# Kernel tuning notes

Hardware: AMD Instinct MI355X
Metric: run time of the kernel (lower is better)

Reference implementation:

```python
import jax, jax.numpy as jnp
import numpy as np

H = 450    # hidden_size (JTNN default)
LAT = 56   # latent_size (tree_vec dim)
V = 780    # vocab size
T = 1024   # n_trees
L = 24     # nodes per tree (path topology)


def _tree_meta(Ln):
    # forward edge i: (i, i+1) eid=i ; reverse edge i: (i+1, i) eid=(Ln-1)+i
    n_f = Ln - 1
    eids, preds, srcs, dsts, labels = [], [], [], [], []
    for i in range(n_f):  # forward DFS steps
        eids.append(i); srcs.append(i); dsts.append(i + 1)
        preds.append(i - 1 if i > 0 else -1); labels.append(0)
    for k in range(n_f):  # backtrack DFS steps (reverse edges, deepest first)
        i = n_f - 1 - k
        eids.append(n_f + i); srcs.append(i + 1); dsts.append(i)
        preds.append(n_f + i + 1 if i < n_f - 1 else -1); labels.append(1)
    # incoming edges of the dst node v (for the node 'pull' h = sum of m)
    in1 = [d - 1 if d > 0 else -1 for d in dsts]
    in2 = [n_f + d if d < n_f else -1 for d in dsts]
    meta = [np.asarray(a, np.int32) for a in (eids, preds, srcs, dsts, in1, in2)]
    return meta, np.asarray(labels, np.float32)


def setup_inputs():
    key = jax.random.key(0)
    ks = jax.random.split(key, 12)
    s = 0.05
    return {
        "wid": jax.random.randint(ks[0], (T, L), 0, V, dtype=jnp.int32),
        "tree_vec": jax.random.normal(ks[1], (T, LAT), jnp.float32),
        "emb": jax.random.normal(ks[2], (V, H)) * s,
        "W_w": jax.random.normal(ks[3], (H + LAT, H)) * s, "W_b": jnp.zeros((H,)),
        "U_w": jax.random.normal(ks[4], (2 * H + LAT, H)) * s, "U_b": jnp.zeros((H,)),
        "Wo_w": jax.random.normal(ks[5], (H, V)) * s, "Wo_b": jnp.zeros((V,)),
        "Us_w": jax.random.normal(ks[6], (H, 1)) * s, "Us_b": jnp.zeros((1,)),
        "Wz_w": jax.random.normal(ks[7], (2 * H, H)) * s, "Wz_b": jnp.zeros((H,)),
        "Wr_w": jax.random.normal(ks[8], (H, H)) * s,
        "Ur_w": jax.random.normal(ks[9], (H, H)) * s, "Ur_b": jnp.zeros((H,)),
        "Wh_w": jax.random.normal(ks[10], (2 * H, H)) * s, "Wh_b": jnp.zeros((H,)),
    }


def reference(wid, tree_vec, emb, W_w, W_b, U_w, U_b, Wo_w, Wo_b, Us_w, Us_b,
              Wz_w, Wz_b, Wr_w, Ur_w, Ur_b, Wh_w, Wh_b):
    Tn, Ln = wid.shape
    n_f = Ln - 1
    nE = 2 * n_f
    meta, labels = _tree_meta(Ln)
    xs = tuple(jnp.asarray(a) for a in meta)
    x = emb[wid]                                  # [T, L, H] node features
    m0 = jnp.zeros((Tn, nE, H), x.dtype)
    rm0 = jnp.zeros((Tn, nE, H), x.dtype)

    def step(carry, sx_):
        m, rm = carry
        eid, pred, src, dst, i1, i2 = sx_
        gp = jnp.maximum(pred, 0)
        s = jnp.where(pred >= 0, m[:, gp], 0.0)        # line-graph pull: sum of m
        arm = jnp.where(pred >= 0, rm[:, gp], 0.0)     # accum_rm
        sxn = x[:, src]                                # src_x
        dxn = x[:, dst]                                # dst_x
        z = jax.nn.sigmoid(jnp.concatenate([sxn, s], 1) @ Wz_w + Wz_b)
        mt = jnp.tanh(jnp.concatenate([sxn, arm], 1) @ Wh_w + Wh_b)
        m_new = (1.0 - z) * s + z * mt
        r = jax.nn.sigmoid(dxn @ Wr_w + m_new @ Ur_w + Ur_b)
        m = m.at[:, eid].set(m_new)
        rm = rm.at[:, eid].set(r * m_new)
        # node pull on v: h_v = sum of m over incoming edges (post edge update)
        h_v = (jnp.where(i1 >= 0, m[:, jnp.maximum(i1, 0)], 0.0)
               + jnp.where(i2 >= 0, m[:, jnp.maximum(i2, 0)], 0.0))
        return (m, rm), (h_v, dxn)

    (_, _), (hs, xvs) = jax.lax.scan(step, (m0, rm0), xs)  # [nE, T, H] each

    tv_steps = jnp.broadcast_to(tree_vec, (nE, Tn, LAT))
    p_in = jnp.concatenate([
        jnp.concatenate([x[:, 0], jnp.zeros((Tn, H), x.dtype), tree_vec], 1),
        jnp.concatenate([xvs, hs, tv_steps], -1).reshape(-1, 2 * H + LAT),
    ], 0)
    q_in = jnp.concatenate([
        jnp.concatenate([jnp.zeros((Tn, H), x.dtype), tree_vec], 1),
        jnp.concatenate([hs[:n_f], tv_steps[:n_f]], -1).reshape(-1, H + LAT),
    ], 0)
    p_targets = jnp.concatenate([jnp.repeat(jnp.asarray(1.0 - labels), Tn),
                                 jnp.zeros((Tn,), jnp.float32)])
    q_targets = wid.T.reshape(-1)

    q_logits = jax.nn.relu(q_in @ W_w + W_b) @ Wo_w + Wo_b
    p_logit = (jax.nn.relu(p_in @ U_w + U_b) @ Us_w + Us_b)[:, 0]
    p_loss = jnp.sum(p_targets * jax.nn.softplus(-p_logit)
                     + (1.0 - p_targets) * jax.nn.softplus(p_logit)) / Tn
    logp = jax.nn.log_softmax(q_logits, -1)
    q_loss = -jnp.sum(jnp.take_along_axis(logp, q_targets[:, None], 1)) / Tn
    p_acc = jnp.mean(((p_logit > 0).astype(jnp.int32) == p_targets.astype(jnp.int32)).astype(jnp.float32))
    q_acc = jnp.mean((jnp.argmax(q_logits, 1) == q_targets).astype(jnp.float32))
    return (q_loss, p_loss, q_acc, p_acc)
```

## Files before the change

kernel.cpp:

```cpp
#include <hip/hip_runtime.h>
#include <hip/hip_bf16.h>
#include <math.h>

#define H 450
#define HP 464
#define KP 480
#define LAT 56
#define V 780
#define LW 24
#define NE 46
#define NF 23
#define SLOT (1024*HP)
#define SROWS 2048
#define QROWS (24*1024)
#define PROWS (47*1024)
#define PTGT  (23*1024)
#define QBLK 6144
#define XBSZ ((size_t)QROWS * H)

typedef __hip_bfloat16 bf16;
typedef __attribute__((ext_vector_type(8))) short short8;
typedef __attribute__((ext_vector_type(4))) float f32x4;

#define MFMA16(a,b,c) __builtin_amdgcn_mfma_f32_16x16x32_bf16(a,b,c,0,0,0)

__device__ __forceinline__ float sigm(float x) { return 1.f / (1.f + expf(-x)); }
__device__ __forceinline__ float toF(bf16 x) { return __bfloat162float(x); }
__device__ __forceinline__ void stV(float* p, float v) { *p = v; }
__device__ __forceinline__ void stV(bf16* p, float v) { *p = __float2bfloat16(v); }
__device__ __forceinline__ short8 ld8(const bf16* p) { return *reinterpret_cast<const short8*>(p); }

__device__ __forceinline__ void gl_lds(const bf16* g, bf16* l) {
    __builtin_amdgcn_global_load_lds(
        (const __attribute__((address_space(1))) void*)g,
        (__attribute__((address_space(3))) void*)l, 16, 0, 0);
}

__device__ __forceinline__ void xcd_decode128(int b, int C, int& row0, int& col0) {
    int rres = b & 7;
    int colt = (b >> 3) % C;
    int g    = b / (8 * C);
    row0 = (rres + 8 * g) * 128;
    col0 = colt * 128;
}
__device__ __forceinline__ void xcd_decode32(int b, int& row0, int& col0) {
    int rres = b & 7;
    int colt = (b >> 3) & 7;
    int g    = b >> 6;
    row0 = (rres + 8 * g) * 32;
    col0 = colt * 64;
}

__global__ __launch_bounds__(256)
void make_bt(const float* __restrict__ src, int K, int N, int ld,
             bf16* __restrict__ dst, int npad) {
    int idx = blockIdx.x * 256 + threadIdx.x;
    if (idx >= npad * KP) return;
    int n = idx / KP, k = idx - n * KP;
    float v = (n < N && k < K) ? src[(size_t)k * ld + n] : 0.f;
    dst[idx] = __float2bfloat16(v);
}

__global__ __launch_bounds__(256)
void pack_bias(const float* __restrict__ zb, const float* __restrict__ hb,
               const float* __restrict__ rb, float* __restrict__ bias4) {
    int i = blockIdx.x * 256 + threadIdx.x;
    if (i >= 1856) return;
    float v = 0.f;
    if (i < 450)       v = zb[i];
    else if (i < 900)  v = hb[i - 450];
    else if (i < 1350) v = rb[i - 900];
    bias4[i] = v;
}

__global__ __launch_bounds__(256)
void zero_init(float* __restrict__ out, float* __restrict__ Sb, int n) {
    int i = blockIdx.x * 256 + threadIdx.x;
    if (i < 4) out[i] = 0.f;
    if (i < n) Sb[i] = 0.f;
}

__global__ __launch_bounds__(256)
void gather_x(const float* __restrict__ emb, const int* __restrict__ wid,
              bf16* __restrict__ x_all) {
    int e = blockIdx.x * 256 + threadIdx.x;
    if (e >= 24 * 1024 * 225) return;
    int row = e / 225, h2 = e - row * 225;
    int t = row >> 10, n = row & 1023;
    int v = wid[n * LW + t];
    float2 x = ((const float2*)(emb + (size_t)v * H))[h2];
    bf16* dst = x_all + (size_t)row * HP + 2 * h2;
    dst[0] = __float2bfloat16(x.x);
    dst[1] = __float2bfloat16(x.y);
}

template<typename TC>
__global__ __launch_bounds__(256)
void gemm128(const bf16* __restrict__ A, int lda,
             const bf16* __restrict__ Bt, int N, int cblk,
             TC* __restrict__ C, int ldc,
             const float* __restrict__ bias,
             const float* __restrict__ addrow, int addld, int relu) {
    __shared__ bf16 As[128 * 32];
    __shared__ bf16 Bs[128 * 32];
    int tid = threadIdx.x;
    int lane = tid & 63, wave = tid >> 6;
    int wx = wave & 1, wy = wave >> 1;
    int lrow = lane & 15, quad = lane >> 4;
    int perm = ((quad + (lrow >> 1)) & 3) * 8;
    int row0, col0;
    xcd_decode128(blockIdx.x, cblk, row0, col0);
    f32x4 acc[4][4] = {};
    for (int k0i = 0; k0i < 15; k0i++) {
        int k0 = k0i * 32;
#pragma unroll
        for (int r = 0; r < 2; r++) {
            int tt = r * 256 + tid;
            int row = tt >> 2, cl = tt & 3;
            int cg = (cl - (row >> 1)) & 3;
            gl_lds(A  + (size_t)(row0 + row) * lda + k0 + cg * 8, As + tt * 8);
            gl_lds(Bt + (size_t)(col0 + row) * KP  + k0 + cg * 8, Bs + tt * 8);
        }
        __syncthreads();
        short8 a[4], b[4];
#pragma unroll
        for (int f = 0; f < 4; f++)
            a[f] = ld8(As + (wy * 64 + f * 16 + lrow) * 32 + perm);
#pragma unroll
        for (int f = 0; f < 4; f++)
            b[f] = ld8(Bs + (wx * 64 + f * 16 + lrow) * 32 + perm);
#pragma unroll
        for (int fi = 0; fi < 4; fi++)
#pragma unroll
            for (int fj = 0; fj < 4; fj++)
                acc[fi][fj] = MFMA16(a[fi], b[fj], acc[fi][fj]);
        __syncthreads();
    }
#pragma unroll
    for (int fi = 0; fi < 4; fi++)
#pragma unroll
        for (int e = 0; e < 4; e++) {
            int r = row0 + wy * 64 + fi * 16 + quad * 4 + e;
#pragma unroll
            for (int fj = 0; fj < 4; fj++) {
                int c = col0 + wx * 64 + fj * 16 + lrow;
                if (c >= N) continue;
                float v = acc[fi][fj][e];
                if (bias) v += bias[c];
                if (addrow) v += addrow[(size_t)(r & 1023) * addld + c];
                if (relu) v = fmaxf(v, 0.f);
                stV(&C[(size_t)r * ldc + c], v);
            }
        }
}

__global__ __launch_bounds__(256)
void gemm128_pre(const bf16* __restrict__ A,
                 const bf16* __restrict__ Bt,
                 bf16* __restrict__ X0,
                 const float* __restrict__ bias4) {
    __shared__ bf16 As[128 * 32];
    __shared__ bf16 Bs[128 * 32];
    int tid = threadIdx.x;
    int lane = tid & 63, wave = tid >> 6;
    int wx = wave & 1, wy = wave >> 1;
    int lrow = lane & 15, quad = lane >> 4;
    int perm = ((quad + (lrow >> 1)) & 3) * 8;
    int row0, col0;
    xcd_decode128(blockIdx.x, 15, row0, col0);
    f32x4 acc[4][4] = {};
    for (int k0i = 0; k0i < 15; k0i++) {
        int k0 = k0i * 32;
#pragma unroll
        for (int r = 0; r < 2; r++) {
            int tt = r * 256 + tid;
            int row = tt >> 2, cl = tt & 3;
            int cg = (cl - (row >> 1)) & 3;
            gl_lds(A  + (size_t)(row0 + row) * HP + k0 + cg * 8, As + tt * 8);
            gl_lds(Bt + (size_t)(col0 + row) * KP + k0 + cg * 8, Bs + tt * 8);
        }
        __syncthreads();
        short8 a[4], b[4];
#pragma unroll
        for (int f = 0; f < 4; f++)
            a[f] = ld8(As + (wy * 64 + f * 16 + lrow) * 32 + perm);
#pragma unroll
        for (int f = 0; f < 4; f++)
            b[f] = ld8(Bs + (wx * 64 + f * 16 + lrow) * 32 + perm);
#pragma unroll
        for (int fi = 0; fi < 4; fi++)
#pragma unroll
            for (int fj = 0; fj < 4; fj++)
                acc[fi][fj] = MFMA16(a[fi], b[fj], acc[fi][fj]);
        __syncthreads();
    }
#pragma unroll
    for (int fi = 0; fi < 4; fi++)
#pragma unroll
        for (int e = 0; e < 4; e++) {
            int r = row0 + wy * 64 + fi * 16 + quad * 4 + e;
#pragma unroll
            for (int fj = 0; fj < 4; fj++) {
                int c = col0 + wx * 64 + fj * 16 + lrow;
                if (c >= 1800) continue;
                int mm = c / 450;
                int cc = c - mm * 450;
                float v = acc[fi][fj][e] + bias4[c];
                X0[(size_t)mm * XBSZ + (size_t)r * H + cc] = __float2bfloat16(v);
            }
        }
}

__global__ __launch_bounds__(256)
void p_gemm128(const bf16* __restrict__ hs, const bf16* __restrict__ UbT,
               const bf16* __restrict__ XUa, const float* __restrict__ Ptv,
               const float* __restrict__ Us, float* __restrict__ pl) {
    __shared__ bf16 As[128 * 32];
    __shared__ bf16 Bs[128 * 32];
    int tid = threadIdx.x;
    int lane = tid & 63, wave = tid >> 6;
    int wx = wave & 1, wy = wave >> 1;
    int lrow = lane & 15, quad = lane >> 4;
    int perm = ((quad + (lrow >> 1)) & 3) * 8;
    int row0, col0;
    xcd_decode128(blockIdx.x, 4, row0, col0);
    f32x4 acc[4][4] = {};
    for (int k0i = 0; k0i < 15; k0i++) {
        int k0 = k0i * 32;
#pragma unroll
        for (int r = 0; r < 2; r++) {
            int tt = r * 256 + tid;
            int row = tt >> 2, cl = tt & 3;
            int cg = (cl - (row >> 1)) & 3;
            gl_lds(hs  + (size_t)(row0 + row) * HP + k0 + cg * 8, As + tt * 8);
            gl_lds(UbT + (size_t)(col0 + row) * KP + k0 + cg * 8, Bs + tt * 8);
        }
        __syncthreads();
        short8 a[4], b[4];
#pragma unroll
        for (int f = 0; f < 4; f++)
            a[f] = ld8(As + (wy * 64 + f * 16 + lrow) * 32 + perm);
#pragma unroll
        for (int f = 0; f < 4; f++)
            b[f] = ld8(Bs + (wx * 64 + f * 16 + lrow) * 32 + perm);
#pragma unroll
        for (int fi = 0; fi < 4; fi++)
#pragma unroll
            for (int fj = 0; fj < 4; fj++)
                acc[fi][fj] = MFMA16(a[fi], b[fj], acc[fi][fj]);
        __syncthreads();
    }
#pragma unroll
    for (int fi = 0; fi < 4; fi++)
#pragma unroll
        for (int e = 0; e < 4; e++) {
            int r = row0 + wy * 64 + fi * 16 + quad * 4 + e;
            int t = r >> 10, n = r & 1023;
            int dst = (t < 23) ? (t + 1) : (45 - t);
            float part = 0.f;
#pragma unroll
            for (int fj = 0; fj < 4; fj++) {
                int c = col0 + wx * 64 + fj * 16 + lrow;
                if (c < H) {
                    float h = fmaxf(acc[fi][fj][e] + toF(XUa[((size_t)dst * 1024 + n) * H + c])
                                    + Ptv[(size_t)n * H + c], 0.f);
                    part += h * Us[c];
                }
            }
#pragma unroll
            for (int off = 1; off < 16; off <<= 1)
                part += __shfl_xor(part, off);
            if (lrow == 0) atomicAdd(&pl[1024 + r], part);
        }
}

__global__ __launch_bounds__(256)
void tv_gemm(const float* __restrict__ tv, const float* __restrict__ Wlat,
             const float* __restrict__ bias, float* __restrict__ out) {
    int n = blockIdx.y;
    int c = blockIdx.x * 256 + threadIdx.x;
    __shared__ float tvs[LAT];
    if (threadIdx.x < LAT) tvs[threadIdx.x] = tv[n * LAT + threadIdx.x];
    __syncthreads();
    if (c < H) {
        float a = bias[c];
#pragma unroll 8
        for (int k = 0; k < LAT; k++) a += tvs[k] * Wlat[(size_t)k * H + c];
        out[(size_t)n * H + c] = a;
    }
}

__global__ __launch_bounds__(256)
void scan_k1(const bf16* __restrict__ AsF, const bf16* __restrict__ AsB,
             const bf16* __restrict__ Arm,
             const bf16* __restrict__ BzT, const bf16* __restrict__ BhT,
             const bf16* __restrict__ Xz, const bf16* __restrict__ Xh,
             float* __restrict__ Sb, bf16* __restrict__ hsF, bf16* __restrict__ hsB,
             int u, int skip) {
    int tid = threadIdx.x;
    int lane = tid & 63, wave = tid >> 6;
    int wx = wave & 1, wy = wave >> 1;
    int lrow = lane & 15, quad = lane >> 4;
    int row0, col0;
    xcd_decode32(blockIdx.x, row0, col0);
    bool fwd = row0 < 1024;
    int rb = row0 & 1023;
    f32x4 az[2] = {}, ah[2] = {};
    if (!skip) {
        const bf16* As = (fwd ? AsF : AsB) + (size_t)(rb + wy * 16 + lrow) * HP + quad * 8;
        const bf16* Ar = Arm + (size_t)(row0 + wy * 16 + lrow) * HP + quad * 8;
        const bf16* bz0 = BzT + (size_t)(col0 + wx * 32 + lrow) * KP + quad * 8;
        const bf16* bh0 = BhT + (size_t)(col0 + wx * 32 + lrow) * KP + quad * 8;
        for (int k = 0; k < 15; k++) {
            short8 s0 = ld8(As + k * 32);
            short8 r0 = ld8(Ar + k * 32);
            short8 z0 = ld8(bz0 + k * 32);
            short8 z1 = ld8(bz0 + 16 * KP + k * 32);
            short8 h0 = ld8(bh0 + k * 32);
            short8 h1 = ld8(bh0 + 16 * KP + k * 32);
            az[0] = MFMA16(s0, z0, az[0]);
            az[1] = MFMA16(s0, z1, az[1]);
            ah[0] = MFMA16(r0, h0, ah[0]);
            ah[1] = MFMA16(r0, h1, ah[1]);
        }
    }
    int src = fwd ? u : 23 - u;
    bf16* hso = fwd ? hsF : hsB;
#pragma unroll
    for (int e = 0; e < 4; e++) {
        int r = row0 + wy * 16 + quad * 4 + e;
        int n = r & 1023;
#pragma unroll
        for (int j = 0; j < 2; j++) {
            int c = col0 + wx * 32 + j * 16 + lrow;
            if (c >= H) continue;
            float zp = az[j][e] + toF(Xz[((size_t)src * 1024 + n) * H + c]);
            float hp = ah[j][e] + toF(Xh[((size_t)src * 1024 + n) * H + c]);
            float s  = Sb[(size_t)r * H + c];
            float z  = sigm(zp);
            float mt = tanhf(hp);
            float mn = (1.f - z) * s + z * mt;
            Sb[(size_t)r * H + c] = mn;
            hso[(size_t)n * HP + c] = __float2bfloat16(mn);
        }
    }
}

__global__ __launch_bounds__(256)
void scan_k2(const bf16* __restrict__ AmF, const bf16* __restrict__ AmB,
             const bf16* __restrict__ UrT, const bf16* __restrict__ Xr,
             const float* __restrict__ Sb, bf16* __restrict__ RMb, int u) {
    int tid = threadIdx.x;
    int lane = tid & 63, wave = tid >> 6;
    int wx = wave & 1, wy = wave >> 1;
    int lrow = lane & 15, quad = lane >> 4;
    int row0, col0;
    xcd_decode32(blockIdx.x, row0, col0);
    bool fwd = row0 < 1024;
    int rb = row0 & 1023;
    const bf16* Am = (fwd ? AmF : AmB) + (size_t)(rb + wy * 16 + lrow) * HP + quad * 8;
    const bf16* b0 = UrT + (size_t)(col0 + wx * 32 + lrow) * KP + quad * 8;
    f32x4 acc[2] = {};
    for (int k = 0; k < 15; k++) {
        short8 a0 = ld8(Am + k * 32);
        short8 w0 = ld8(b0 + k * 32);
        short8 w1 = ld8(b0 + 16 * KP + k * 32);
        acc[0] = MFMA16(a0, w0, acc[0]);
        acc[1] = MFMA16(a0, w1, acc[1]);
    }
    int dst = fwd ? (u + 1) : (22 - u);
#pragma unroll
    for (int e = 0; e < 4; e++) {
        int r = row0 + wy * 16 + quad * 4 + e;
        int n = r & 1023;
#pragma unroll
        for (int j = 0; j < 2; j++) {
            int c = col0 + wx * 32 + j * 16 + lrow;
            if (c >= H) continue;
            float rp = acc[j][e] + toF(Xr[((size_t)dst * 1024 + n) * H + c]);
            float rr = sigm(rp);
            RMb[(size_t)r * HP + c] = __float2bfloat16(rr * Sb[(size_t)r * H + c]);
        }
    }
}

__global__ __launch_bounds__(256)
void hv_fixup(bf16* __restrict__ hs) {
    int idx = blockIdx.x * 256 + threadIdx.x;
    if (idx >= 22 * SLOT) return;
    int tl = idx / SLOT;
    int rem = idx - tl * SLOT;
    size_t a = (size_t)(23 + tl) * SLOT + rem;
    size_t b = (size_t)(21 - tl) * SLOT + rem;
    hs[a] = __float2bfloat16(toF(hs[a]) + toF(hs[b]));
}

__global__ __launch_bounds__(256)
void q_root(const float* __restrict__ Qtv, bf16* __restrict__ qh) {
    int idx = blockIdx.x * 256 + threadIdx.x;
    if (idx >= 1024 * H) return;
    int n = idx / H, c = idx - n * H;
    qh[(size_t)n * HP + c] = __float2bfloat16(fmaxf(Qtv[idx], 0.f));
}

__global__ __launch_bounds__(256)
void q_reduce(const float* __restrict__ ql, const int* __restrict__ wid,
              float* __restrict__ qred) {
    int wave = threadIdx.x >> 6, lane = threadIdx.x & 63;
    int r = blockIdx.x * 4 + wave;
    int t = r >> 10, n = r & 1023;
    int tgt = wid[n * LW + t];
    const float4* row4 = (const float4*)(ql + (size_t)r * V);
    float m = -3.4e38f, s = 0.f; int mi = 0x7fffffff;
#pragma unroll
    for (int k = 0; k < 4; k++) {
        int c4 = lane + 64 * k;
        if (c4 < 195) {
            float4 v4 = row4[c4];
            float vv[4] = {v4.x, v4.y, v4.z, v4.w};
#pragma unroll
            for (int e = 0; e < 4; e++) {
                float v = vv[e];
                if (v > m) { s = s * __expf(m - v) + 1.f; m = v; mi = c4 * 4 + e; }
                else s += __expf(v - m);
            }
        }
    }
#pragma unroll
    for (int off = 1; off < 64; off <<= 1) {
        float m2 = __shfl_xor(m, off);
        float s2 = __shfl_xor(s, off);
        int   i2 = __shfl_xor(mi, off);
        if (m2 > m || (m2 == m && i2 < mi)) {
            s = s2 + s * __expf(m - m2);
            m = m2; mi = i2;
        } else {
            s = s + s2 * __expf(m2 - m);
        }
    }
    __shared__ float lred[4][2];
    if (lane == 0) {
        float lse = m + logf(s);
        lred[wave][0] = lse - ql[(size_t)r * V + tgt];
        lred[wave][1] = (mi == tgt) ? 1.f : 0.f;
    }
    __syncthreads();
    if (threadIdx.x == 0) {
        qred[blockIdx.x * 2]     = lred[0][0] + lred[1][0] + lred[2][0] + lred[3][0];
        qred[blockIdx.x * 2 + 1] = lred[0][1] + lred[1][1] + lred[2][1] + lred[3][1];
    }
}

__global__ __launch_bounds__(256)
void q_final(const float* __restrict__ qred, float* __restrict__ out) {
    int tid = threadIdx.x;
    float L = 0.f, A = 0.f;
    for (int i = tid; i < QBLK; i += 256) { L += qred[2 * i]; A += qred[2 * i + 1]; }
    __shared__ float s1[256], s2[256];
    s1[tid] = L; s2[tid] = A;
    __syncthreads();
    for (int k = 128; k > 0; k >>= 1) {
        if (tid < k) { s1[tid] += s1[tid + k]; s2[tid] += s2[tid + k]; }
        __syncthreads();
    }
    if (tid == 0) {
        out[0] = s1[0] * (1.f / 1024.f);
        out[2] = s2[0] * (1.f / 24576.f);
    }
}

__global__ __launch_bounds__(256)
void p_init(float* __restrict__ pl, const float* __restrict__ Us_b) {
    int idx = blockIdx.x * 256 + threadIdx.x;
    if (idx < PROWS) pl[idx] = Us_b[0];
}

__global__ __launch_bounds__(256)
void p_root(const bf16* __restrict__ XUa, const float* __restrict__ Ptv,
            const float* __restrict__ Us, float* __restrict__ pl) {
    int n = blockIdx.x;
    int tid = threadIdx.x;
    const bf16* xa = XUa + (size_t)n * H;
    const float* pt = Ptv + (size_t)n * H;
    float s = 0.f;
    for (int c = tid; c < H; c += 256)
        s += fmaxf(toF(xa[c]) + pt[c], 0.f) * Us[c];
    __shared__ float red[256];
    red[tid] = s;
    __syncthreads();
    for (int k = 128; k > 0; k >>= 1) {
        if (tid < k) red[tid] += red[tid + k];
        __syncthreads();
    }
    if (tid == 0) atomicAdd(&pl[n], red[0]);
}

__global__ __launch_bounds__(256)
void p_final(const float* __restrict__ pl, float* __restrict__ out) {
    int r = blockIdx.x * 256 + threadIdx.x;
    int tid = threadIdx.x;
    float loss = 0.f, acc = 0.f;
    if (r < PROWS) {
        float l = pl[r];
        int tgt = (r < PTGT) ? 1 : 0;
        float x = tgt ? -l : l;
        loss = fmaxf(x, 0.f) + log1pf(expf(-fabsf(x)));
        int pred = (l > 0.f) ? 1 : 0;
        acc = (pred == tgt) ? 1.f : 0.f;
    }
    __shared__ float s1[256], s2[256];
    s1[tid] = loss; s2[tid] = acc;
    __syncthreads();
    for (int k = 128; k > 0; k >>= 1) {
        if (tid < k) { s1[tid] += s1[tid + k]; s2[tid] += s2[tid + k]; }
        __syncthreads();
    }
    if (tid == 0) {
        atomicAdd(&out[1], s1[0] * (1.f / 1024.f));
        atomicAdd(&out[3], s2[0] * (1.f / 48128.f));
    }
}

extern "C" void kernel_launch(void* const* d_in, const int* in_sizes, int n_in,
                              void* d_out, int out_size, void* d_ws, size_t ws_size,
                              hipStream_t stream) {
    const int*   wid  = (const int*)  d_in[0];
    const float* tv   = (const float*)d_in[1];
    const float* emb  = (const float*)d_in[2];
    const float* W_w  = (const float*)d_in[3];
    const float* W_b  = (const float*)d_in[4];
    const float* U_w  = (const float*)d_in[5];
    const float* U_b  = (const float*)d_in[6];
    const float* Wo_w = (const float*)d_in[7];
    const float* Wo_b = (const float*)d_in[8];
    const float* Us_w = (const float*)d_in[9];
    const float* Us_b = (const float*)d_in[10];
    const float* Wz_w = (const float*)d_in[11];
    const float* Wz_b = (const float*)d_in[12];
    const float* Wr_w = (const float*)d_in[13];
    const float* Ur_w = (const float*)d_in[14];
    const float* Ur_b = (const float*)d_in[15];
    const float* Wh_w = (const float*)d_in[16];
    const float* Wh_b = (const float*)d_in[17];
    float* out = (float*)d_out;

    char* base = (char*)d_ws;
    const size_t XBb = XBSZ * 2;
    bf16*  Xz   = (bf16*)(base);
    bf16*  Xh   = (bf16*)(base + XBb);
    bf16*  Xr   = (bf16*)(base + 2 * XBb);
    bf16*  XUa  = (bf16*)(base + 3 * XBb);
    bf16*  hs   = (bf16*)(base + 4 * XBb);
    bf16*  x_all = hs;
    char*  p1   = base + 4 * XBb + (size_t)NE * SLOT * 2;
    bf16*  RMb  = (bf16*)p1;                p1 += (size_t)SROWS * HP * 2;
    float* Sb   = (float*)p1;               p1 += (size_t)SROWS * H * 4;
    float* Qtv  = (float*)p1;               p1 += (size_t)1024 * H * 4;
    float* Ptv  = (float*)p1;               p1 += (size_t)1024 * H * 4;
    float* pl   = (float*)p1;               p1 += (size_t)PROWS * 4;
    float* qred = (float*)p1;               p1 += (size_t)QBLK * 2 * 4;
    float* bias4 = (float*)p1;              p1 += (size_t)1856 * 4;
    bf16*  BT   = (bf16*)p1;
    bf16* BT4   = BT;
    bf16* WzbT  = BT + (size_t)1856 * KP;
    bf16* WhbT  = WzbT + (size_t)512 * KP;
    bf16* UrT   = WhbT + (size_t)512 * KP;
    bf16* UbT   = UrT  + (size_t)512 * KP;
    bf16* WtopT = UbT  + (size_t)512 * KP;
    bf16* WoT   = WtopT + (size_t)512 * KP;
    bf16*  qh = (bf16*)base;
    float* ql = (float*)(base + (size_t)QROWS * HP * 2);

    zero_init<<<(SROWS * H + 255) / 256, 256, 0, stream>>>(out, Sb, SROWS * H);
    int btg = (512 * KP + 255) / 256;
    int btg450 = (450 * KP + 255) / 256;
    make_bt<<<btg450, 256, 0, stream>>>(Wz_w, H, H, H, BT4,                        450);
    make_bt<<<btg450, 256, 0, stream>>>(Wh_w, H, H, H, BT4 + (size_t)450 * KP,     450);
    make_bt<<<btg450, 256, 0, stream>>>(Wr_w, H, H, H, BT4 + (size_t)900 * KP,     450);
    make_bt<<<(506 * KP + 255) / 256, 256, 0, stream>>>(U_w, H, H, H, BT4 + (size_t)1350 * KP, 506);
    pack_bias<<<8, 256, 0, stream>>>(Wz_b, Wh_b, Ur_b, bias4);
    make_bt<<<btg, 256, 0, stream>>>(Wz_w + 450*450,  H, H, H, WzbT, 512);
    make_bt<<<btg, 256, 0, stream>>>(Wh_w + 450*450,  H, H, H, WhbT, 512);
    make_bt<<<btg, 256, 0, stream>>>(Ur_w,            H, H, H, UrT,  512);
    make_bt<<<btg, 256, 0, stream>>>(U_w + 450*450,   H, H, H, UbT,  512);
    make_bt<<<btg, 256, 0, stream>>>(W_w,             H, H, H, WtopT, 512);
    make_bt<<<(896 * KP + 255) / 256, 256, 0, stream>>>(Wo_w, H, V, V, WoT, 896);

    gather_x<<<(24 * 1024 * 225 + 255) / 256, 256, 0, stream>>>(emb, wid, x_all);
    gemm128_pre<<<(QROWS / 128) * 15, 256, 0, stream>>>(x_all, BT4, Xz, bias4);

    tv_gemm<<<dim3(2, 1024), 256, 0, stream>>>(tv, W_w + 450*450, W_b, Qtv);
    tv_gemm<<<dim3(2, 1024), 256, 0, stream>>>(tv, U_w + 900*450, U_b, Ptv);

    for (int u = 0; u < 23; u++) {
        const bf16* AsF = hs + (size_t)(u - 1) * SLOT;
        const bf16* AsB = hs + (size_t)(22 + u) * SLOT;
        scan_k1<<<512, 256, 0, stream>>>(AsF, AsB, RMb, WzbT, WhbT, Xz, Xh,
                                         Sb, hs + (size_t)u * SLOT,
                                         hs + (size_t)(23 + u) * SLOT, u, u == 0 ? 1 : 0);
        if (u < 22)
            scan_k2<<<512, 256, 0, stream>>>(hs + (size_t)u * SLOT, hs + (size_t)(23 + u) * SLOT,
                                             UrT, Xr, Sb, RMb, u);
    }
    hv_fixup<<<(22 * SLOT + 255) / 256, 256, 0, stream>>>(hs);

    p_init<<<(PROWS + 255) / 256, 256, 0, stream>>>(pl, Us_b);
    p_root<<<1024, 256, 0, stream>>>(XUa, Ptv, Us_w, pl);
    p_gemm128<<<(PROWS - 1024) / 128 * 4, 256, 0, stream>>>(hs, UbT, XUa, Ptv, Us_w, pl);
    p_final<<<PROWS / 256, 256, 0, stream>>>(pl, out);

    q_root<<<(1024 * H + 255) / 256, 256, 0, stream>>>(Qtv, qh);
    gemm128<bf16><<<(NF * 1024 / 128) * 4, 256, 0, stream>>>(hs, HP, WtopT, H, 4,
                                                             qh + (size_t)1024 * HP, HP,
                                                             (const float*)nullptr, Qtv, H, 1);
    gemm128<float><<<(QROWS / 128) * 7, 256, 0, stream>>>(qh, HP, WoT, V, 7, ql, V,
                                                          Wo_b, (const float*)nullptr, H, 0);
    q_reduce<<<QBLK, 256, 0, stream>>>(ql, wid, qred);
    q_final<<<1, 256, 0, stream>>>(qred, out);

    (void)in_sizes; (void)n_in; (void)out_size; (void)ws_size;
}
```

Measured before the change: 1.091 ms.

## Fuse the 45 per-step GRU scan launches into one persistent kernel

Replaces the 23-step host loop of scan_k1/scan_k2 launches with a single kernel. Each block owns 16 tree rows for all time steps and keeps the GRU state in registers and the bf16 message/reset tiles in LDS, so the per-step launches and the Sb/RMb global round trips go away. The trade-off is parallelism: only 128 blocks of 256 threads do the whole recurrence, and each block re-reads the full Wz/Wh/Ur weight matrices from global/L2 at every step.

```diff
diff --git a/kernel.cpp b/kernel.cpp
--- a/kernel.cpp
+++ b/kernel.cpp
@@ -43,13 +43,6 @@
     row0 = (rres + 8 * g) * 128;
     col0 = colt * 128;
 }
-__device__ __forceinline__ void xcd_decode32(int b, int& row0, int& col0) {
-    int rres = b & 7;
-    int colt = (b >> 3) & 7;
-    int g    = b >> 6;
-    row0 = (rres + 8 * g) * 32;
-    col0 = colt * 64;
-}
 
 __global__ __launch_bounds__(256)
 void make_bt(const float* __restrict__ src, int K, int N, int ld,
@@ -74,10 +67,9 @@
 }
 
 __global__ __launch_bounds__(256)
-void zero_init(float* __restrict__ out, float* __restrict__ Sb, int n) {
-    int i = blockIdx.x * 256 + threadIdx.x;
+void zero_init(float* __restrict__ out) {
+    int i = threadIdx.x;
     if (i < 4) out[i] = 0.f;
-    if (i < n) Sb[i] = 0.f;
 }
 
 __global__ __launch_bounds__(256)
@@ -291,95 +283,106 @@
 }
 
 __global__ __launch_bounds__(256)
-void scan_k1(const bf16* __restrict__ AsF, const bf16* __restrict__ AsB,
-             const bf16* __restrict__ Arm,
-             const bf16* __restrict__ BzT, const bf16* __restrict__ BhT,
-             const bf16* __restrict__ Xz, const bf16* __restrict__ Xh,
-             float* __restrict__ Sb, bf16* __restrict__ hsF, bf16* __restrict__ hsB,
-             int u, int skip) {
+void scan_full(bf16* __restrict__ hs,
+               const bf16* __restrict__ WzbT, const bf16* __restrict__ WhbT,
+               const bf16* __restrict__ UrT,
+               const bf16* __restrict__ Xz, const bf16* __restrict__ Xh,
+               const bf16* __restrict__ Xr) {
+    __shared__ bf16 mnl[2][16][488];
+    __shared__ bf16 rml[16][488];
     int tid = threadIdx.x;
-    int lane = tid & 63, wave = tid >> 6;
-    int wx = wave & 1, wy = wave >> 1;
+    int lane = tid & 63, w = tid >> 6;
     int lrow = lane & 15, quad = lane >> 4;
-    int row0, col0;
-    xcd_decode32(blockIdx.x, row0, col0);
+    int row0 = blockIdx.x * 16;
     bool fwd = row0 < 1024;
-    int rb = row0 & 1023;
-    f32x4 az[2] = {}, ah[2] = {};
-    if (!skip) {
-        const bf16* As = (fwd ? AsF : AsB) + (size_t)(rb + wy * 16 + lrow) * HP + quad * 8;
-        const bf16* Ar = Arm + (size_t)(row0 + wy * 16 + lrow) * HP + quad * 8;
-        const bf16* bz0 = BzT + (size_t)(col0 + wx * 32 + lrow) * KP + quad * 8;
-        const bf16* bh0 = BhT + (size_t)(col0 + wx * 32 + lrow) * KP + quad * 8;
-        for (int k = 0; k < 15; k++) {
-            short8 s0 = ld8(As + k * 32);
-            short8 r0 = ld8(Ar + k * 32);
-            short8 z0 = ld8(bz0 + k * 32);
-            short8 z1 = ld8(bz0 + 16 * KP + k * 32);
-            short8 h0 = ld8(bh0 + k * 32);
-            short8 h1 = ld8(bh0 + 16 * KP + k * 32);
-            az[0] = MFMA16(s0, z0, az[0]);
-            az[1] = MFMA16(s0, z1, az[1]);
-            ah[0] = MFMA16(r0, h0, ah[0]);
-            ah[1] = MFMA16(r0, h1, ah[1]);
-        }
-    }
-    int src = fwd ? u : 23 - u;
-    bf16* hso = fwd ? hsF : hsB;
-#pragma unroll
-    for (int e = 0; e < 4; e++) {
-        int r = row0 + wy * 16 + quad * 4 + e;
-        int n = r & 1023;
-#pragma unroll
-        for (int j = 0; j < 2; j++) {
-            int c = col0 + wx * 32 + j * 16 + lrow;
-            if (c >= H) continue;
-            float zp = az[j][e] + toF(Xz[((size_t)src * 1024 + n) * H + c]);
-            float hp = ah[j][e] + toF(Xh[((size_t)src * 1024 + n) * H + c]);
-            float s  = Sb[(size_t)r * H + c];
-            float z  = sigm(zp);
-            float mt = tanhf(hp);
-            float mn = (1.f - z) * s + z * mt;
-            Sb[(size_t)r * H + c] = mn;
-            hso[(size_t)n * HP + c] = __float2bfloat16(mn);
-        }
-    }
-}
-
-__global__ __launch_bounds__(256)
-void scan_k2(const bf16* __restrict__ AmF, const bf16* __restrict__ AmB,
-             const bf16* __restrict__ UrT, const bf16* __restrict__ Xr,
-             const float* __restrict__ Sb, bf16* __restrict__ RMb, int u) {
-    int tid = threadIdx.x;
-    int lane = tid & 63, wave = tid >> 6;
-    int wx = wave & 1, wy = wave >> 1;
-    int lrow = lane & 15, quad = lane >> 4;
-    int row0, col0;
-    xcd_decode32(blockIdx.x, row0, col0);
-    bool fwd = row0 < 1024;
-    int rb = row0 & 1023;
-    const bf16* Am = (fwd ? AmF : AmB) + (size_t)(rb + wy * 16 + lrow) * HP + quad * 8;
-    const bf16* b0 = UrT + (size_t)(col0 + wx * 32 + lrow) * KP + quad * 8;
-    f32x4 acc[2] = {};
-    for (int k = 0; k < 15; k++) {
-        short8 a0 = ld8(Am + k * 32);
-        short8 w0 = ld8(b0 + k * 32);
-        short8 w1 = ld8(b0 + 16 * KP + k * 32);
-        acc[0] = MFMA16(a0, w0, acc[0]);
-        acc[1] = MFMA16(a0, w1, acc[1]);
-    }
-    int dst = fwd ? (u + 1) : (22 - u);
-#pragma unroll
-    for (int e = 0; e < 4; e++) {
-        int r = row0 + wy * 16 + quad * 4 + e;
-        int n = r & 1023;
-#pragma unroll
-        for (int j = 0; j < 2; j++) {
-            int c = col0 + wx * 32 + j * 16 + lrow;
-            if (c >= H) continue;
-            float rp = acc[j][e] + toF(Xr[((size_t)dst * 1024 + n) * H + c]);
-            float rr = sigm(rp);
-            RMb[(size_t)r * HP + c] = __float2bfloat16(rr * Sb[(size_t)r * H + c]);
+    float sreg[8][4];
+#pragma unroll
+    for (int i = 0; i < 8; i++)
+#pragma unroll
+        for (int e = 0; e < 4; e++) sreg[i][e] = 0.f;
+    for (int i = tid; i < 2 * 16 * 488; i += 256) ((bf16*)mnl)[i] = __float2bfloat16(0.f);
+    for (int i = tid; i < 16 * 488; i += 256) ((bf16*)rml)[i] = __float2bfloat16(0.f);
+    __syncthreads();
+
+    for (int u = 0; u < 23; u++) {
+        int cur = u & 1, prev = cur ^ 1;
+        f32x4 az[8], ah[8];
+#pragma unroll
+        for (int i = 0; i < 8; i++) {
+            az[i] = (f32x4){0.f, 0.f, 0.f, 0.f};
+            ah[i] = (f32x4){0.f, 0.f, 0.f, 0.f};
+        }
+        if (u > 0) {
+            for (int k = 0; k < 15; k++) {
+                short8 sA = *reinterpret_cast<const short8*>(&mnl[prev][lrow][k * 32 + quad * 8]);
+                short8 rA = *reinterpret_cast<const short8*>(&rml[lrow][k * 32 + quad * 8]);
+#pragma unroll
+                for (int i = 0; i < 8; i++) {
+                    int f = w + 4 * i;
+                    if (f >= 29) break;
+                    short8 zB = ld8(WzbT + (size_t)(f * 16 + lrow) * KP + k * 32 + quad * 8);
+                    short8 hB = ld8(WhbT + (size_t)(f * 16 + lrow) * KP + k * 32 + quad * 8);
+                    az[i] = MFMA16(sA, zB, az[i]);
+                    ah[i] = MFMA16(rA, hB, ah[i]);
+                }
+            }
+        }
+        int src = fwd ? u : 23 - u;
+        bf16* hso = hs + (size_t)(fwd ? u : 23 + u) * SLOT;
+#pragma unroll
+        for (int i = 0; i < 8; i++) {
+            int f = w + 4 * i;
+            if (f >= 29) break;
+            int c = f * 16 + lrow;
+            if (c < H) {
+#pragma unroll
+                for (int e = 0; e < 4; e++) {
+                    int rl = quad * 4 + e;
+                    int n = (row0 + rl) & 1023;
+                    float zp = az[i][e] + toF(Xz[((size_t)src * 1024 + n) * H + c]);
+                    float hp = ah[i][e] + toF(Xh[((size_t)src * 1024 + n) * H + c]);
+                    float z = sigm(zp), mt = tanhf(hp);
+                    float mn = (1.f - z) * sreg[i][e] + z * mt;
+                    sreg[i][e] = mn;
+                    bf16 mb = __float2bfloat16(mn);
+                    mnl[cur][rl][c] = mb;
+                    hso[(size_t)n * HP + c] = mb;
+                }
+            }
+        }
+        __syncthreads();
+
+        if (u < 22) {
+            f32x4 ar[8];
+#pragma unroll
+            for (int i = 0; i < 8; i++) ar[i] = (f32x4){0.f, 0.f, 0.f, 0.f};
+            for (int k = 0; k < 15; k++) {
+                short8 a = *reinterpret_cast<const short8*>(&mnl[cur][lrow][k * 32 + quad * 8]);
+#pragma unroll
+                for (int i = 0; i < 8; i++) {
+                    int f = w + 4 * i;
+                    if (f >= 29) break;
+                    short8 b = ld8(UrT + (size_t)(f * 16 + lrow) * KP + k * 32 + quad * 8);
+                    ar[i] = MFMA16(a, b, ar[i]);
+                }
+            }
+            int dst = fwd ? (u + 1) : (22 - u);
+#pragma unroll
+            for (int i = 0; i < 8; i++) {
+                int f = w + 4 * i;
+                if (f >= 29) break;
+                int c = f * 16 + lrow;
+                if (c < H) {
+#pragma unroll
+                    for (int e = 0; e < 4; e++) {
+                        int rl = quad * 4 + e;
+                        int n = (row0 + rl) & 1023;
+                        float rp = ar[i][e] + toF(Xr[((size_t)dst * 1024 + n) * H + c]);
+                        rml[rl][c] = __float2bfloat16(sigm(rp) * toF(mnl[cur][rl][c]));
+                    }
+                }
+            }
+            __syncthreads();
         }
     }
 }
@@ -553,8 +556,6 @@
     bf16*  hs   = (bf16*)(base + 4 * XBb);
     bf16*  x_all = hs;
     char*  p1   = base + 4 * XBb + (size_t)NE * SLOT * 2;
-    bf16*  RMb  = (bf16*)p1;                p1 += (size_t)SROWS * HP * 2;
-    float* Sb   = (float*)p1;               p1 += (size_t)SROWS * H * 4;
     float* Qtv  = (float*)p1;               p1 += (size_t)1024 * H * 4;
     float* Ptv  = (float*)p1;               p1 += (size_t)1024 * H * 4;
     float* pl   = (float*)p1;               p1 += (size_t)PROWS * 4;
@@ -571,7 +572,7 @@
     bf16*  qh = (bf16*)base;
     float* ql = (float*)(base + (size_t)QROWS * HP * 2);
 
-    zero_init<<<(SROWS * H + 255) / 256, 256, 0, stream>>>(out, Sb, SROWS * H);
+    zero_init<<<1, 256, 0, stream>>>(out);
     int btg = (512 * KP + 255) / 256;
     int btg450 = (450 * KP + 255) / 256;
     make_bt<<<btg450, 256, 0, stream>>>(Wz_w, H, H, H, BT4,                        450);
@@ -592,16 +593,7 @@
     tv_gemm<<<dim3(2, 1024), 256, 0, stream>>>(tv, W_w + 450*450, W_b, Qtv);
     tv_gemm<<<dim3(2, 1024), 256, 0, stream>>>(tv, U_w + 900*450, U_b, Ptv);
 
-    for (int u = 0; u < 23; u++) {
-        const bf16* AsF = hs + (size_t)(u - 1) * SLOT;
-        const bf16* AsB = hs + (size_t)(22 + u) * SLOT;
-        scan_k1<<<512, 256, 0, stream>>>(AsF, AsB, RMb, WzbT, WhbT, Xz, Xh,
-                                         Sb, hs + (size_t)u * SLOT,
-                                         hs + (size_t)(23 + u) * SLOT, u, u == 0 ? 1 : 0);
-        if (u < 22)
-            scan_k2<<<512, 256, 0, stream>>>(hs + (size_t)u * SLOT, hs + (size_t)(23 + u) * SLOT,
-                                             UrT, Xr, Sb, RMb, u);
-    }
+    scan_full<<<SROWS / 16, 256, 0, stream>>>(hs, WzbT, WhbT, UrT, Xz, Xh, Xr);
     hv_fixup<<<(22 * SLOT + 255) / 256, 256, 0, stream>>>(hs);
 
     p_init<<<(PROWS + 255) / 256, 256, 0, stream>>>(pl, Us_b);
```

After: 1.706 ms. 1.56x slower.
